# Performance work log

Measured on AMD Instinct MI355X. Metric: run time of the kernel, lower is better.

## Reference

```python
import jax, jax.numpy as jnp
import numpy as np

PARAM = 10.0
EPS = 1e-10

def delu(x):
    # delu_feature_map: param*relu(x) + (exp(param*min(x,0)) - 1) + 1
    return PARAM * jax.nn.relu(x) + jnp.expm1(PARAM * jnp.minimum(x, 0.0)) + 1.0

def conv1x1(x, w, b):
    # x: (B,C,H,W), w: (O,C), b: (O,)
    return jnp.einsum('oc,bchw->bohw', w, x) + b[None, :, None, None]

def conv3x3(x, w, b):
    # x: (B,C,H,W), w: (O,C,3,3)
    y = jax.lax.conv_general_dilated(x, w, window_strides=(1, 1), padding='SAME',
                                     dimension_numbers=('NCHW', 'OIHW', 'NCHW'))
    return y + b[None, :, None, None]

def setup_inputs() -> dict:
    key = jax.random.key(0)
    B, C, H, W = 4, 256, 128, 128
    ks = jax.random.split(key, 20)
    s = 0.05
    d = {
        'x1': jax.random.normal(ks[0], (B, C, H, W), jnp.float32),
        'x2': jax.random.normal(ks[1], (B, C, H, W), jnp.float32),
        'wq1': jax.random.normal(ks[2], (C, C), jnp.float32) * s,
        'bq1': jax.random.normal(ks[3], (C,), jnp.float32) * s,
        'wk1': jax.random.normal(ks[4], (C, C), jnp.float32) * s,
        'bk1': jax.random.normal(ks[5], (C,), jnp.float32) * s,
        'wv1': jax.random.normal(ks[6], (C, C), jnp.float32) * s,
        'bv1': jax.random.normal(ks[7], (C,), jnp.float32) * s,
        'wq2': jax.random.normal(ks[8], (C, C), jnp.float32) * s,
        'bq2': jax.random.normal(ks[9], (C,), jnp.float32) * s,
        'wk2': jax.random.normal(ks[10], (C, C), jnp.float32) * s,
        'bk2': jax.random.normal(ks[11], (C,), jnp.float32) * s,
        'wv2': jax.random.normal(ks[12], (C, C), jnp.float32) * s,
        'bv2': jax.random.normal(ks[13], (C,), jnp.float32) * s,
        'wd1': jax.random.normal(ks[14], (C, C), jnp.float32) * s,
        'bd1': jax.random.normal(ks[15], (C,), jnp.float32) * s,
        'wd3': jax.random.normal(ks[16], (C, C, 3, 3), jnp.float32) * s,
        'bd3': jax.random.normal(ks[17], (C,), jnp.float32) * s,
        'gamma1': jax.random.normal(ks[18], (1,), jnp.float32) * 0.5,
        'gamma2': jax.random.normal(ks[19], (1,), jnp.float32) * 0.5,
    }
    return d

def reference(x1, x2, wq1, bq1, wk1, bk1, wv1, bv1, wq2, bq2, wk2, bk2,
              wv2, bv2, wd1, bd1, wd3, bd3, gamma1, gamma2):
    B, C, H, W = x1.shape
    N = H * W
    # QKV projections (1x1 convs), flattened to (B,C,N). delu is elementwise,
    # so applying it on (B,C,N) equals the permute/delu/permute in torch.
    q1 = delu(conv1x1(x1, wq1, bq1).reshape(B, C, N))
    k1 = delu(conv1x1(x1, wk1, bk1).reshape(B, C, N))
    v1 = conv1x1(x1, wv1, bv1).reshape(B, C, N)
    q2 = delu(conv1x1(x2, wq2, bq2).reshape(B, C, N))
    k2 = delu(conv1x1(x2, wk2, bk2).reshape(B, C, N))
    v2 = conv1x1(x2, wv2, bv2).reshape(B, C, N)

    # energy: (B,C,C) cross-kernel matrices
    energy1 = jnp.einsum('bmn,bcn->bmc', q1, k2)
    energy2 = jnp.einsum('bmn,bcn->bmc', q2, k1)

    KV1 = k1 * v1  # (B,C,N)
    KV2 = k2 * v2

    # norm: 1 / (sum_{m,c} energy[b,m,c] * k[b,c,n] + eps) -> (B,N)
    esum1 = energy1.sum(axis=1)  # (B,C)
    esum2 = energy2.sum(axis=1)
    norm1 = 1.0 / (jnp.einsum('bc,bcn->bn', esum1, k2) + EPS)
    norm2 = 1.0 / (jnp.einsum('bc,bcn->bn', esum2, k1) + EPS)

    # einsum('bmc,bcn,bn->bcn') factorizes: sum over m hits only energy
    att1 = (esum1[:, :, None] * KV1 * norm1[:, None, :]).reshape(B, C, H, W)
    att2 = (esum2[:, :, None] * KV2 * norm2[:, None, :]).reshape(B, C, H, W)

    out1 = att1 + conv1x1(x1, wd1, bd1) + conv3x3(x1, wd3, bd3)
    out2 = att2 + conv1x1(x2, wd1, bd1) + conv3x3(x2, wd3, bd3)
    out1 = x1 + gamma1[0] * out1
    out2 = x2 + gamma2[0] * out2
    return (out1, out2)
```

## Files before the change

kernel.cpp:

```cpp
#include <hip/hip_runtime.h>
#include <stdint.h>

#define Bn 4
#define Cn 256
#define Hn 128
#define Wn 128
#define Nn 16384
#define EPSn 1e-10f

typedef unsigned short u16;
typedef __attribute__((ext_vector_type(8))) short short8;
typedef __attribute__((ext_vector_type(4))) short short4v;
typedef __attribute__((ext_vector_type(4))) float f32x4;

#define GLOAD_LDS16(g, l)                                                        \
    __builtin_amdgcn_global_load_lds(                                            \
        (const __attribute__((address_space(1))) unsigned int*)(const void*)(g), \
        (__attribute__((address_space(3))) unsigned int*)(void*)(l), 16, 0, 0)

#define MFMA16(a, b, c) __builtin_amdgcn_mfma_f32_16x16x32_bf16(a, b, c, 0, 0, 0)

__device__ __forceinline__ float bf2f(u16 u) {
    union { float f; uint32_t i; } v; v.i = ((uint32_t)u) << 16; return v.f;
}
__device__ __forceinline__ u16 f2bf(float f) {
    union { float f; uint32_t i; } v; v.f = f;
    uint32_t r = v.i + 0x7FFFu + ((v.i >> 16) & 1u);
    return (u16)(r >> 16);
}
__device__ __forceinline__ float delu_f(float x) {
    return x >= 0.f ? fmaf(10.f, x, 1.f) : __expf(10.f * x);
}

__global__ void prep_kernel(const float* __restrict__ wq1, const float* __restrict__ wk1,
                            const float* __restrict__ wv1,
                            const float* __restrict__ wq2, const float* __restrict__ wk2,
                            const float* __restrict__ wv2,
                            const float* __restrict__ wd1, const float* __restrict__ wd3,
                            const float* __restrict__ bd1, const float* __restrict__ bd3,
                            const float* __restrict__ gamma1, const float* __restrict__ gamma2,
                            u16* __restrict__ wq1p, u16* __restrict__ wk1p, u16* __restrict__ wv1p,
                            u16* __restrict__ wq2p, u16* __restrict__ wk2p, u16* __restrict__ wv2p,
                            u16* __restrict__ wallp1, u16* __restrict__ wallp2,
                            float* __restrict__ bfused)
{
    int idx = blockIdx.x * 256 + threadIdx.x;
    int o = idx >> 8, c = idx & 255;
    if (idx < 256) bfused[idx] = bd1[idx] + bd3[idx];
    int s = o >> 6, mf = (o >> 4) & 3, lr = o & 15;
    int kc = c >> 5, lk = (c >> 3) & 3, j = c & 7;
    int poff = ((kc * 4 + s) * 4 + mf) * 512 + (lk * 16 + lr) * 8 + j;
    wq1p[poff] = f2bf(wq1[idx]);
    wk1p[poff] = f2bf(wk1[idx]);
    wv1p[poff] = f2bf(wv1[idx]);
    wq2p[poff] = f2bf(wq2[idx]);
    wk2p[poff] = f2bf(wk2[idx]);
    wv2p[poff] = f2bf(wv2[idx]);
    float wd1v = wd1[idx];
    float inv1 = 1.f / gamma1[0];
    float inv2 = 1.f / gamma2[0];
    float diag = (o == c) ? 1.f : 0.f;
    #pragma unroll
    for (int tap = 0; tap < 9; ++tap) {
        float w = wd3[idx * 9 + tap] + (tap == 4 ? wd1v : 0.f);
        wallp1[tap * 65536 + poff] = f2bf(w + (tap == 4 ? diag * inv1 : 0.f));
        wallp2[tap * 65536 + poff] = f2bf(w + (tap == 4 ? diag * inv2 : 0.f));
    }
}

__global__ void transpose_kernel(const float* __restrict__ x1, const float* __restrict__ x2,
                                 u16* __restrict__ xT1, u16* __restrict__ xT2)
{
    __shared__ __align__(16) u16 tl[64][72];
    int t = threadIdx.x;
    int z = blockIdx.z, img = z >> 2, b = z & 3;
    const float* x = img ? x2 : x1;
    u16* xT = img ? xT2 : xT1;
    int n0 = blockIdx.x * 64, c0 = blockIdx.y * 64;
    int cl = t >> 4, nl = (t & 15) * 4;
    #pragma unroll
    for (int pc = 0; pc < 4; ++pc) {
        int c = pc * 16 + cl;
        float4 v = *(const float4*)&x[((size_t)(b * Cn + c0 + c)) * Nn + n0 + nl];
        tl[nl + 0][c] = f2bf(v.x);
        tl[nl + 1][c] = f2bf(v.y);
        tl[nl + 2][c] = f2bf(v.z);
        tl[nl + 3][c] = f2bf(v.w);
    }
    __syncthreads();
    #pragma unroll
    for (int ps = 0; ps < 2; ++ps) {
        int id = ps * 256 + t;
        int nr = id >> 3, cc = (id & 7) * 8;
        short8 v = *(const short8*)&tl[nr][cc];
        *(short8*)&xT[((size_t)(b * Nn + n0 + nr)) * 256 + c0 + cc] = v;
    }
}

#define QK_LDS (2 * 128 * 68)

__global__ __launch_bounds__(256, 3) void qkv_kernel(
    const u16* __restrict__ xT1, const u16* __restrict__ xT2,
    const u16* __restrict__ wq1p, const u16* __restrict__ wk1p, const u16* __restrict__ wv1p,
    const u16* __restrict__ wq2p, const u16* __restrict__ wk2p, const u16* __restrict__ wv2p,
    const float* __restrict__ bq1, const float* __restrict__ bk1, const float* __restrict__ bv1,
    const float* __restrict__ bq2, const float* __restrict__ bk2, const float* __restrict__ bv2,
    u16* __restrict__ k1, u16* __restrict__ k2,
    u16* __restrict__ kv1, u16* __restrict__ kv2,
    float* __restrict__ qsum1, float* __restrict__ qsum2)
{
    __shared__ __align__(16) u16 lds[QK_LDS];
    int t = threadIdx.x;
    int nb = blockIdx.x, mb = blockIdx.y;
    int z = blockIdx.z, img = z >> 2, b = z & 3;
    const u16* xT  = img ? xT2  : xT1;
    const u16* wqp = img ? wq2p : wq1p;
    const u16* wkp = img ? wk2p : wk1p;
    const u16* wvp = img ? wv2p : wv1p;
    const float* bq = img ? bq2 : bq1;
    const float* bk = img ? bk2 : bk1;
    const float* bv = img ? bv2 : bv1;
    u16* kout  = img ? k2  : k1;
    u16* kvout = img ? kv2 : kv1;
    float* qsum = img ? qsum2 : qsum1;

    int n0 = nb * 64;
    int lane = t & 63, wid = t >> 6;
    int wm = wid >> 1, wn = wid & 1;
    int lr = lane & 15, lk = lane >> 4;
    int s = mb * 2 + wm;

    f32x4 zf = {0.f, 0.f, 0.f, 0.f};
    f32x4 accq[4][2], acck[4][2], accv[4][2];
    #pragma unroll
    for (int i = 0; i < 4; ++i)
        #pragma unroll
        for (int j = 0; j < 2; ++j) { accq[i][j] = zf; acck[i][j] = zf; accv[i][j] = zf; }

    int colp = lane >> 2, chp = (lane & 3) * 8;
    #pragma unroll
    for (int kc = 0; kc < 8; ++kc) {
        const u16* g = xT + ((size_t)(b * Nn + n0 + wid * 16 + colp)) * 256 + kc * 32 + chp;
        GLOAD_LDS16(g, &lds[kc * 2048 + (wid * 16) * 32]);
    }
    __syncthreads();

    #pragma unroll
    for (int kc = 0; kc < 8; ++kc) {
        int abase = ((kc * 4 + s) * 4) * 512 + lane * 8;
        short8 bf0 = *(const short8*)&lds[kc * 2048 + (wn * 32 + 0 * 16 + lr) * 32 + lk * 8];
        short8 bf1 = *(const short8*)&lds[kc * 2048 + (wn * 32 + 1 * 16 + lr) * 32 + lk * 8];
        #pragma unroll
        for (int mf = 0; mf < 4; ++mf) {
            short8 aq = *(const short8*)&wqp[abase + mf * 512];
            short8 ak = *(const short8*)&wkp[abase + mf * 512];
            short8 av = *(const short8*)&wvp[abase + mf * 512];
            __builtin_amdgcn_s_setprio(1);
            accq[mf][0] = MFMA16(aq, bf0, accq[mf][0]);
            accq[mf][1] = MFMA16(aq, bf1, accq[mf][1]);
            acck[mf][0] = MFMA16(ak, bf0, acck[mf][0]);
            acck[mf][1] = MFMA16(ak, bf1, acck[mf][1]);
            accv[mf][0] = MFMA16(av, bf0, accv[mf][0]);
            accv[mf][1] = MFMA16(av, bf1, accv[mf][1]);
            __builtin_amdgcn_s_setprio(0);
        }
    }
    __syncthreads();

    float qs[2] = {0.f, 0.f};
    #pragma unroll
    for (int mf = 0; mf < 4; ++mf) {
        #pragma unroll
        for (int r = 0; r < 4; ++r) {
            int o = mb * 128 + wm * 64 + mf * 16 + lk * 4 + r;
            float bqv = bq[o];
            #pragma unroll
            for (int nf = 0; nf < 2; ++nf)
                qs[nf] += delu_f(accq[mf][nf][r] + bqv);
        }
    }
    #pragma unroll
    for (int nf = 0; nf < 2; ++nf) {
        float sgl = qs[nf];
        sgl += __shfl_xor(sgl, 16);
        sgl += __shfl_xor(sgl, 32);
        if (lk == 0)
            atomicAdd(&qsum[b * Nn + n0 + wn * 32 + nf * 16 + lr], sgl);
    }

    #pragma unroll
    for (int mf = 0; mf < 4; ++mf) {
        #pragma unroll
        for (int r = 0; r < 4; ++r) {
            int ol = wm * 64 + mf * 16 + lk * 4 + r;
            float bkv = bk[mb * 128 + ol];
            float bvv = bv[mb * 128 + ol];
            #pragma unroll
            for (int nf = 0; nf < 2; ++nf) {
                float kk = delu_f(acck[mf][nf][r] + bkv);
                float vv = accv[mf][nf][r] + bvv;
                int col = wn * 32 + nf * 16 + lr;
                lds[ol * 68 + col] = f2bf(kk);
                lds[128 * 68 + ol * 68 + col] = f2bf(kk * vv);
            }
        }
    }
    __syncthreads();

    #pragma unroll
    for (int i = 0; i < 4; ++i) {
        int sid = i * 256 + t;
        int o = sid >> 3, seg = sid & 7;
        short8 v = *(const short8*)&lds[o * 68 + seg * 8];
        *(short8*)&kout[((size_t)(b * Cn + mb * 128 + o)) * Nn + n0 + seg * 8] = v;
    }
    #pragma unroll
    for (int i = 0; i < 4; ++i) {
        int sid = i * 256 + t;
        int o = sid >> 3, seg = sid & 7;
        short8 v = *(const short8*)&lds[128 * 68 + o * 68 + seg * 8];
        *(short8*)&kvout[((size_t)(b * Cn + mb * 128 + o)) * Nn + n0 + seg * 8] = v;
    }
}

__global__ void esum_kernel(const u16* __restrict__ k1, const u16* __restrict__ k2,
                            const float* __restrict__ qsum1, const float* __restrict__ qsum2,
                            float* __restrict__ esum1, float* __restrict__ esum2)
{
    int c = blockIdx.x, b = blockIdx.y, pair = blockIdx.z, t = threadIdx.x;
    const u16* k = pair ? k1 : k2;
    const float* qsum = pair ? qsum2 : qsum1;
    float* esum = pair ? esum2 : esum1;
    const u16* kr = k + ((size_t)(b * Cn + c)) * Nn;
    const float* qr = qsum + b * Nn;
    float s = 0.f;
    for (int i = t * 8; i < Nn; i += 2048) {
        short8 kv = *(const short8*)&kr[i];
        #pragma unroll
        for (int j = 0; j < 8; ++j) s = fmaf(bf2f((u16)kv[j]), qr[i + j], s);
    }
    #pragma unroll
    for (int m = 32; m; m >>= 1) s += __shfl_xor(s, m);
    __shared__ float red[4];
    if ((t & 63) == 0) red[t >> 6] = s;
    __syncthreads();
    if (t == 0) esum[b * Cn + c] = red[0] + red[1] + red[2] + red[3];
}

__global__ void norm_kernel(const u16* __restrict__ k1, const u16* __restrict__ k2,
                            const float* __restrict__ esum1, const float* __restrict__ esum2,
                            float* __restrict__ norm1, float* __restrict__ norm2)
{
    __shared__ float es[256];
    int t = threadIdx.x, b = blockIdx.y, pair = blockIdx.z;
    const u16* k = pair ? k1 : k2;
    const float* esum = pair ? esum2 : esum1;
    float* nrm = pair ? norm2 : norm1;
    es[t] = esum[b * Cn + t];
    __syncthreads();
    int n = blockIdx.x * 256 + t;
    const u16* kb = k + (size_t)b * Cn * Nn + n;
    float a = 0.f;
    #pragma unroll 8
    for (int c = 0; c < 256; ++c)
        a = fmaf(es[c], bf2f(kb[(size_t)c * Nn]), a);
    nrm[b * Nn + n] = 1.f / (a + EPSn);
}

#define BSZ6 (6 * 130 * 32)

__global__ __launch_bounds__(512, 2) void conv_att_kernel(
    const u16* __restrict__ xT,
    const u16* __restrict__ wallp, const float* __restrict__ bfused,
    const u16* __restrict__ kv, const float* __restrict__ esum,
    const float* __restrict__ nrm, const float* __restrict__ gamma,
    float* __restrict__ out)
{
    __shared__ __align__(16) u16 Bl[2 * BSZ6];
    int t = threadIdx.x;
    int lin = (blockIdx.z * 32 + blockIdx.y) * 2 + blockIdx.x;
    int xcd = lin & 7, slot = lin >> 3;
    int b = xcd >> 1;
    int ys = (xcd & 1) * 16 + (slot >> 1);
    int mb = slot & 1;
    int ybase = ys * 4;
    int lane = t & 63, wid = t >> 6;
    int wm = wid & 1, wy = wid >> 1;
    int lr = lane & 15, lk = lane >> 4;
    int s = mb * 2 + wm;

    f32x4 zf = {0.f, 0.f, 0.f, 0.f};
    f32x4 acc[4][8];
    #pragma unroll
    for (int i = 0; i < 4; ++i)
        #pragma unroll
        for (int j = 0; j < 8; ++j) acc[i][j] = zf;

    if (t < 96) {
        int buf = t / 48, r = t % 48;
        int row = r >> 3, pos = ((r >> 2) & 1) ? 129 : 0, q = r & 3;
        short8 z = {0, 0, 0, 0, 0, 0, 0, 0};
        *(short8*)&Bl[buf * BSZ6 + (row * 130 + pos) * 32 + q * 8] = z;
    }

    int colp = lane >> 2, chp = (lane & 3) * 8;
    auto STAGE = [&](int bufi, int kc) {
        #pragma unroll
        for (int i = 0; i < 6; ++i) {
            int run = wid * 6 + i;
            int hy = run >> 3, sx = run & 7;
            int yy = ybase + hy - 1;
            int dst = bufi * BSZ6 + (hy * 130 + 1 + sx * 16) * 32;
            if (yy < 0 || yy >= Hn) {
                short8 z = {0, 0, 0, 0, 0, 0, 0, 0};
                *(short8*)&Bl[dst + lane * 8] = z;
            } else {
                const u16* g = xT + ((size_t)(b * Nn + yy * Wn + sx * 16 + colp)) * 256
                                  + kc * 32 + chp;
                GLOAD_LDS16(g, &Bl[dst]);
            }
        }
    };

    STAGE(0, 0);
    __syncthreads();

    for (int kc = 0; kc < 8; ++kc) {
        int cur = kc & 1;
        int abase = ((kc * 4 + s) * 4) * 512 + lane * 8;
        short8 af[3][4];
        #pragma unroll
        for (int mf = 0; mf < 4; ++mf)
            af[0][mf] = *(const short8*)&wallp[0 * 65536 + abase + mf * 512];
        #pragma unroll
        for (int mf = 0; mf < 4; ++mf)
            af[1][mf] = *(const short8*)&wallp[1 * 65536 + abase + mf * 512];
        if (kc < 7) STAGE(cur ^ 1, kc + 1);
        int cb = cur * BSZ6;
        #pragma unroll
        for (int tap = 0; tap < 9; ++tap) {
            if (tap < 7) {
                #pragma unroll
                for (int mf = 0; mf < 4; ++mf)
                    af[(tap + 2) % 3][mf] =
                        *(const short8*)&wallp[(tap + 2) * 65536 + abase + mf * 512];
            }
            int dy = tap / 3, dx = tap % 3;
            short8 bf[8];
            #pragma unroll
            for (int nf = 0; nf < 8; ++nf)
                bf[nf] = *(const short8*)&Bl[cb + ((wy + dy) * 130 + nf * 16 + lr + dx) * 32 + lk * 8];
            __builtin_amdgcn_s_setprio(1);
            #pragma unroll
            for (int mf = 0; mf < 4; ++mf) {
                #pragma unroll
                for (int nf = 0; nf < 8; ++nf)
                    acc[mf][nf] = MFMA16(af[tap % 3][mf], bf[nf], acc[mf][nf]);
            }
            __builtin_amdgcn_s_setprio(0);
        }
        __syncthreads();
    }

    float g = gamma[0];
    int y = ybase + wy;
    int nbase = y * Wn;
    float nr8[8];
    #pragma unroll
    for (int nf = 0; nf < 8; ++nf)
        nr8[nf] = nrm[b * Nn + nbase + nf * 16 + lr];
    #pragma unroll
    for (int mf = 0; mf < 4; ++mf) {
        #pragma unroll
        for (int r = 0; r < 4; ++r) {
            int o = mb * 128 + wm * 64 + mf * 16 + lk * 4 + r;
            float es_o = esum[b * Cn + o];
            float bf_o = bfused[o];
            size_t rowbase = ((size_t)(b * Cn + o)) * Nn + nbase;
            #pragma unroll
            for (int nf = 0; nf < 8; ++nf) {
                size_t idx = rowbase + nf * 16 + lr;
                float att = es_o * bf2f(kv[idx]) * nr8[nf];
                out[idx] = g * (acc[mf][nf][r] + bf_o + att);
            }
        }
    }
}

extern "C" void kernel_launch(void* const* d_in, const int* in_sizes, int n_in,
                              void* d_out, int out_size, void* d_ws, size_t ws_size,
                              hipStream_t stream)
{
    const float* x1  = (const float*)d_in[0];
    const float* x2  = (const float*)d_in[1];
    const float* wq1 = (const float*)d_in[2];
    const float* bq1 = (const float*)d_in[3];
    const float* wk1 = (const float*)d_in[4];
    const float* bk1 = (const float*)d_in[5];
    const float* wv1 = (const float*)d_in[6];
    const float* bv1 = (const float*)d_in[7];
    const float* wq2 = (const float*)d_in[8];
    const float* bq2 = (const float*)d_in[9];
    const float* wk2 = (const float*)d_in[10];
    const float* bk2 = (const float*)d_in[11];
    const float* wv2 = (const float*)d_in[12];
    const float* bv2 = (const float*)d_in[13];
    const float* wd1 = (const float*)d_in[14];
    const float* bd1 = (const float*)d_in[15];
    const float* wd3 = (const float*)d_in[16];
    const float* bd3 = (const float*)d_in[17];
    const float* gamma1 = (const float*)d_in[18];
    const float* gamma2 = (const float*)d_in[19];

    char* ws = (char*)d_ws;
    size_t off = 0;
    auto alloc = [&](size_t bytes) { char* p = ws + off; off += (bytes + 255) & ~(size_t)255; return p; };

    u16* xT1    = (u16*)alloc((size_t)Bn * Nn * Cn * 2);
    u16* xT2    = (u16*)alloc((size_t)Bn * Nn * Cn * 2);
    u16* k1     = (u16*)alloc((size_t)Bn * Cn * Nn * 2);
    u16* k2     = (u16*)alloc((size_t)Bn * Cn * Nn * 2);
    u16* kv2    = (u16*)alloc((size_t)Bn * Cn * Nn * 2);
    u16* wallp1 = (u16*)alloc((size_t)9 * 65536 * 2);
    u16* wallp2 = (u16*)alloc((size_t)9 * 65536 * 2);
    u16* wq1p   = (u16*)alloc(65536 * 2);
    u16* wk1p   = (u16*)alloc(65536 * 2);
    u16* wv1p   = (u16*)alloc(65536 * 2);
    u16* wq2p   = (u16*)alloc(65536 * 2);
    u16* wk2p   = (u16*)alloc(65536 * 2);
    u16* wv2p   = (u16*)alloc(65536 * 2);
    float* qsum1 = (float*)alloc(Bn * Nn * 4);
    float* qsum2 = (float*)alloc(Bn * Nn * 4);
    float* esum1 = (float*)alloc(Bn * Cn * 4);
    float* esum2 = (float*)alloc(Bn * Cn * 4);
    float* norm1 = (float*)alloc(Bn * Nn * 4);
    float* norm2 = (float*)alloc(Bn * Nn * 4);
    float* bfused = (float*)alloc(Cn * 4);

    float* out1 = (float*)d_out;
    float* out2 = out1 + (size_t)Bn * Cn * Nn;
    u16* kv1 = (u16*)out2;

    hipMemsetAsync(qsum1, 0, Bn * Nn * 4, stream);
    hipMemsetAsync(qsum2, 0, Bn * Nn * 4, stream);

    prep_kernel<<<dim3(256), dim3(256), 0, stream>>>(wq1, wk1, wv1, wq2, wk2, wv2, wd1, wd3,
                                                     bd1, bd3, gamma1, gamma2,
                                                     wq1p, wk1p, wv1p, wq2p, wk2p, wv2p,
                                                     wallp1, wallp2, bfused);
    transpose_kernel<<<dim3(256, 4, 8), 256, 0, stream>>>(x1, x2, xT1, xT2);
    qkv_kernel<<<dim3(256, 2, 8), 256, 0, stream>>>(xT1, xT2,
                                                    wq1p, wk1p, wv1p, wq2p, wk2p, wv2p,
                                                    bq1, bk1, bv1, bq2, bk2, bv2,
                                                    k1, k2, kv1, kv2, qsum1, qsum2);
    esum_kernel<<<dim3(256, 4, 2), 256, 0, stream>>>(k1, k2, qsum1, qsum2, esum1, esum2);
    norm_kernel<<<dim3(64, 4, 2), 256, 0, stream>>>(k1, k2, esum1, esum2, norm1, norm2);
    conv_att_kernel<<<dim3(2, 32, 4), 512, 0, stream>>>(xT1, wallp1, bfused, kv1,
                                                        esum1, norm1, gamma1, out1);
    conv_att_kernel<<<dim3(2, 32, 4), 512, 0, stream>>>(xT2, wallp2, bfused, kv2,
                                                        esum2, norm2, gamma2, out2);
}
```

Before: 332.1 us.

## Split QKV projection across six waves, one wave pair per Q, K, V

The QKV kernel grows from 4 to 6 waves per block. Each pair of waves now computes a single projection (Q, K or V) over the full 64-column tile, where before every wave computed all three projections over half the columns. Each wave loads one weight stream instead of three and keeps a 4x4 accumulator tile, which is meant to cut register pressure and raise MFMA parallelism per block. In exchange, the K*V product now goes through LDS with an extra barrier, and the LDS row stride changes to 72.

```diff
diff --git a/kernel.cpp b/kernel.cpp
--- a/kernel.cpp
+++ b/kernel.cpp
@@ -97,9 +97,10 @@
     }
 }
 
-#define QK_LDS (2 * 128 * 68)
-
-__global__ __launch_bounds__(256, 3) void qkv_kernel(
+#define OSTR 72
+#define QK_LDS (2 * 128 * OSTR)
+
+__global__ __launch_bounds__(384, 3) void qkv_kernel(
     const u16* __restrict__ xT1, const u16* __restrict__ xT2,
     const u16* __restrict__ wq1p, const u16* __restrict__ wk1p, const u16* __restrict__ wv1p,
     const u16* __restrict__ wq2p, const u16* __restrict__ wk2p, const u16* __restrict__ wv2p,
@@ -126,100 +127,122 @@
 
     int n0 = nb * 64;
     int lane = t & 63, wid = t >> 6;
-    int wm = wid >> 1, wn = wid & 1;
+    int wg = wid >> 1;
+    int wm = wid & 1;
     int lr = lane & 15, lk = lane >> 4;
     int s = mb * 2 + wm;
+    const u16* wsel = (wg == 0) ? wqp : ((wg == 1) ? wkp : wvp);
 
     f32x4 zf = {0.f, 0.f, 0.f, 0.f};
-    f32x4 accq[4][2], acck[4][2], accv[4][2];
+    f32x4 acc[4][4];
     #pragma unroll
     for (int i = 0; i < 4; ++i)
         #pragma unroll
-        for (int j = 0; j < 2; ++j) { accq[i][j] = zf; acck[i][j] = zf; accv[i][j] = zf; }
+        for (int j = 0; j < 4; ++j) acc[i][j] = zf;
 
     int colp = lane >> 2, chp = (lane & 3) * 8;
-    #pragma unroll
-    for (int kc = 0; kc < 8; ++kc) {
-        const u16* g = xT + ((size_t)(b * Nn + n0 + wid * 16 + colp)) * 256 + kc * 32 + chp;
-        GLOAD_LDS16(g, &lds[kc * 2048 + (wid * 16) * 32]);
+    for (int i = wid; i < 32; i += 6) {
+        int kc = i >> 2, seg = i & 3;
+        const u16* g = xT + ((size_t)(b * Nn + n0 + seg * 16 + colp)) * 256 + kc * 32 + chp;
+        GLOAD_LDS16(g, &lds[kc * 2048 + (seg * 16) * 32]);
     }
     __syncthreads();
 
     #pragma unroll
     for (int kc = 0; kc < 8; ++kc) {
         int abase = ((kc * 4 + s) * 4) * 512 + lane * 8;
-        short8 bf0 = *(const short8*)&lds[kc * 2048 + (wn * 32 + 0 * 16 + lr) * 32 + lk * 8];
-        short8 bf1 = *(const short8*)&lds[kc * 2048 + (wn * 32 + 1 * 16 + lr) * 32 + lk * 8];
+        short8 a0 = *(const short8*)&wsel[abase + 0 * 512];
+        short8 a1 = *(const short8*)&wsel[abase + 1 * 512];
+        short8 a2 = *(const short8*)&wsel[abase + 2 * 512];
+        short8 a3 = *(const short8*)&wsel[abase + 3 * 512];
+        short8 bf0 = *(const short8*)&lds[kc * 2048 + (0 * 16 + lr) * 32 + lk * 8];
+        short8 bf1 = *(const short8*)&lds[kc * 2048 + (1 * 16 + lr) * 32 + lk * 8];
+        short8 bf2 = *(const short8*)&lds[kc * 2048 + (2 * 16 + lr) * 32 + lk * 8];
+        short8 bf3 = *(const short8*)&lds[kc * 2048 + (3 * 16 + lr) * 32 + lk * 8];
+        __builtin_amdgcn_s_setprio(1);
+        acc[0][0] = MFMA16(a0, bf0, acc[0][0]); acc[0][1] = MFMA16(a0, bf1, acc[0][1]);
+        acc[0][2] = MFMA16(a0, bf2, acc[0][2]); acc[0][3] = MFMA16(a0, bf3, acc[0][3]);
+        acc[1][0] = MFMA16(a1, bf0, acc[1][0]); acc[1][1] = MFMA16(a1, bf1, acc[1][1]);
+        acc[1][2] = MFMA16(a1, bf2, acc[1][2]); acc[1][3] = MFMA16(a1, bf3, acc[1][3]);
+        acc[2][0] = MFMA16(a2, bf0, acc[2][0]); acc[2][1] = MFMA16(a2, bf1, acc[2][1]);
+        acc[2][2] = MFMA16(a2, bf2, acc[2][2]); acc[2][3] = MFMA16(a2, bf3, acc[2][3]);
+        acc[3][0] = MFMA16(a3, bf0, acc[3][0]); acc[3][1] = MFMA16(a3, bf1, acc[3][1]);
+        acc[3][2] = MFMA16(a3, bf2, acc[3][2]); acc[3][3] = MFMA16(a3, bf3, acc[3][3]);
+        __builtin_amdgcn_s_setprio(0);
+    }
+    __syncthreads();
+
+    if (wg == 0) {
+        float qs[4] = {0.f, 0.f, 0.f, 0.f};
         #pragma unroll
         for (int mf = 0; mf < 4; ++mf) {
-            short8 aq = *(const short8*)&wqp[abase + mf * 512];
-            short8 ak = *(const short8*)&wkp[abase + mf * 512];
-            short8 av = *(const short8*)&wvp[abase + mf * 512];
-            __builtin_amdgcn_s_setprio(1);
-            accq[mf][0] = MFMA16(aq, bf0, accq[mf][0]);
-            accq[mf][1] = MFMA16(aq, bf1, accq[mf][1]);
-            acck[mf][0] = MFMA16(ak, bf0, acck[mf][0]);
-            acck[mf][1] = MFMA16(ak, bf1, acck[mf][1]);
-            accv[mf][0] = MFMA16(av, bf0, accv[mf][0]);
-            accv[mf][1] = MFMA16(av, bf1, accv[mf][1]);
-            __builtin_amdgcn_s_setprio(0);
-        }
-    }
-    __syncthreads();
-
-    float qs[2] = {0.f, 0.f};
-    #pragma unroll
-    for (int mf = 0; mf < 4; ++mf) {
-        #pragma unroll
-        for (int r = 0; r < 4; ++r) {
-            int o = mb * 128 + wm * 64 + mf * 16 + lk * 4 + r;
-            float bqv = bq[o];
-            #pragma unroll
-            for (int nf = 0; nf < 2; ++nf)
-                qs[nf] += delu_f(accq[mf][nf][r] + bqv);
-        }
-    }
-    #pragma unroll
-    for (int nf = 0; nf < 2; ++nf) {
-        float sgl = qs[nf];
-        sgl += __shfl_xor(sgl, 16);
-        sgl += __shfl_xor(sgl, 32);
-        if (lk == 0)
-            atomicAdd(&qsum[b * Nn + n0 + wn * 32 + nf * 16 + lr], sgl);
-    }
-
-    #pragma unroll
-    for (int mf = 0; mf < 4; ++mf) {
-        #pragma unroll
-        for (int r = 0; r < 4; ++r) {
-            int ol = wm * 64 + mf * 16 + lk * 4 + r;
-            float bkv = bk[mb * 128 + ol];
-            float bvv = bv[mb * 128 + ol];
-            #pragma unroll
-            for (int nf = 0; nf < 2; ++nf) {
-                float kk = delu_f(acck[mf][nf][r] + bkv);
-                float vv = accv[mf][nf][r] + bvv;
-                int col = wn * 32 + nf * 16 + lr;
-                lds[ol * 68 + col] = f2bf(kk);
-                lds[128 * 68 + ol * 68 + col] = f2bf(kk * vv);
-            }
-        }
-    }
-    __syncthreads();
-
-    #pragma unroll
-    for (int i = 0; i < 4; ++i) {
-        int sid = i * 256 + t;
-        int o = sid >> 3, seg = sid & 7;
-        short8 v = *(const short8*)&lds[o * 68 + seg * 8];
-        *(short8*)&kout[((size_t)(b * Cn + mb * 128 + o)) * Nn + n0 + seg * 8] = v;
-    }
-    #pragma unroll
-    for (int i = 0; i < 4; ++i) {
-        int sid = i * 256 + t;
-        int o = sid >> 3, seg = sid & 7;
-        short8 v = *(const short8*)&lds[128 * 68 + o * 68 + seg * 8];
-        *(short8*)&kvout[((size_t)(b * Cn + mb * 128 + o)) * Nn + n0 + seg * 8] = v;
+            #pragma unroll
+            for (int r = 0; r < 4; ++r) {
+                int o = mb * 128 + wm * 64 + mf * 16 + lk * 4 + r;
+                float bqv = bq[o];
+                #pragma unroll
+                for (int nf = 0; nf < 4; ++nf)
+                    qs[nf] += delu_f(acc[mf][nf][r] + bqv);
+            }
+        }
+        #pragma unroll
+        for (int nf = 0; nf < 4; ++nf) {
+            float sgl = qs[nf];
+            sgl += __shfl_xor(sgl, 16);
+            sgl += __shfl_xor(sgl, 32);
+            if (lk == 0)
+                atomicAdd(&qsum[b * Nn + n0 + nf * 16 + lr], sgl);
+        }
+    } else if (wg == 1) {
+        #pragma unroll
+        for (int mf = 0; mf < 4; ++mf) {
+            #pragma unroll
+            for (int r = 0; r < 4; ++r) {
+                int ol = wm * 64 + mf * 16 + lk * 4 + r;
+                float bkv = bk[mb * 128 + ol];
+                #pragma unroll
+                for (int nf = 0; nf < 4; ++nf)
+                    lds[ol * OSTR + nf * 16 + lr] = f2bf(delu_f(acc[mf][nf][r] + bkv));
+            }
+        }
+    }
+    __syncthreads();
+
+    if (wg == 2) {
+        #pragma unroll
+        for (int mf = 0; mf < 4; ++mf) {
+            #pragma unroll
+            for (int r = 0; r < 4; ++r) {
+                int ol = wm * 64 + mf * 16 + lk * 4 + r;
+                float bvv = bv[mb * 128 + ol];
+                #pragma unroll
+                for (int nf = 0; nf < 4; ++nf) {
+                    float kk = bf2f(lds[ol * OSTR + nf * 16 + lr]);
+                    float vv = acc[mf][nf][r] + bvv;
+                    lds[128 * OSTR + ol * OSTR + nf * 16 + lr] = f2bf(kk * vv);
+                }
+            }
+        }
+    }
+    __syncthreads();
+
+    #pragma unroll
+    for (int i = 0; i < 3; ++i) {
+        int sid = i * 384 + t;
+        if (sid < 1024) {
+            int o = sid >> 3, seg = sid & 7;
+            short8 v = *(const short8*)&lds[o * OSTR + seg * 8];
+            *(short8*)&kout[((size_t)(b * Cn + mb * 128 + o)) * Nn + n0 + seg * 8] = v;
+        }
+    }
+    #pragma unroll
+    for (int i = 0; i < 3; ++i) {
+        int sid = i * 384 + t;
+        if (sid < 1024) {
+            int o = sid >> 3, seg = sid & 7;
+            short8 v = *(const short8*)&lds[128 * OSTR + o * OSTR + seg * 8];
+            *(short8*)&kvout[((size_t)(b * Cn + mb * 128 + o)) * Nn + n0 + seg * 8] = v;
+        }
     }
 }
 
@@ -449,7 +472,7 @@
                                                      wq1p, wk1p, wv1p, wq2p, wk2p, wv2p,
                                                      wallp1, wallp2, bfused);
     transpose_kernel<<<dim3(256, 4, 8), 256, 0, stream>>>(x1, x2, xT1, xT2);
-    qkv_kernel<<<dim3(256, 2, 8), 256, 0, stream>>>(xT1, xT2,
+    qkv_kernel<<<dim3(256, 2, 8), 384, 0, stream>>>(xT1, xT2,
                                                     wq1p, wk1p, wv1p, wq2p, wk2p, wv2p,
                                                     bq1, bk1, bv1, bq2, bk2, bv2,
                                                     k1, k2, kv1, kv2, qsum1, qsum2);
```

Measured after the change: 365.2 us. 1.1x slower.
